# Performance work log

Measured on AMD Instinct MI355X. Metric: run time of the kernel, lower is better.

Reference implementation:

```python
import jax, jax.numpy as jnp
import numpy as np

N = 100000          # nodes
E = 1600000         # edges (avg degree 16)
F_IN = 128          # node_feature_dim
D = 64              # state_dim
LATENT = 32         # latent_dim -> output 2*latent
ROUNDS = 4


def setup_inputs() -> dict:
    key = jax.random.key(0)
    ks = jax.random.split(key, 12)
    s = 0.05  # weight scale
    return {
        "x": jax.random.normal(ks[0], (N, F_IN), dtype=jnp.float32),
        "edge_index": jax.random.randint(ks[1], (2, E), 0, N, dtype=jnp.int64),
        "batch": jnp.zeros((N,), dtype=jnp.int64),
        # input MLP: Linear(F_IN, D) + ReLU + Linear(D, D) + ReLU
        "W1": jax.random.normal(ks[2], (F_IN, D), dtype=jnp.float32) * s,
        "b1": jnp.zeros((D,), dtype=jnp.float32),
        "W2": jax.random.normal(ks[3], (D, D), dtype=jnp.float32) * s,
        "b2": jnp.zeros((D,), dtype=jnp.float32),
        # per-round GraphConv params (PyG: lin_rel has bias, lin_root does not)
        "Wrel": jax.random.normal(ks[4], (ROUNDS, D, D), dtype=jnp.float32) * s,
        "brel": jnp.zeros((ROUNDS, D), dtype=jnp.float32),
        "Wroot": jax.random.normal(ks[5], (ROUNDS, D, D), dtype=jnp.float32) * s,
        # output Linear(D, 2*latent)
        "Wout": jax.random.normal(ks[6], (D, 2 * LATENT), dtype=jnp.float32) * s,
        "bout": jnp.zeros((2 * LATENT,), dtype=jnp.float32),
    }


def reference(x, edge_index, batch, W1, b1, W2, b2, Wrel, brel, Wroot, Wout, bout):
    # input MLP (ends with ReLU) followed by the extra F.relu in forward (idempotent, kept for fidelity)
    h = jax.nn.relu(x @ W1 + b1)
    h = jax.nn.relu(h @ W2 + b2)
    h = jax.nn.relu(h)
    src, dst = edge_index[0], edge_index[1]
    n = h.shape[0]
    num_rounds = Wrel.shape[0]
    for r in range(num_rounds):
        # GraphConv: scatter-add of source features to destinations, then lin_rel + lin_root
        agg = jax.ops.segment_sum(h[src], dst, num_segments=n)  # [N, D]
        conv = agg @ Wrel[r] + brel[r] + h @ Wroot[r]
        h = h + jax.nn.relu(conv)  # residual
    return h @ Wout + bout  # [N, 2*latent]
```

## Files before the change

kernel.cpp:

```cpp
#include <hip/hip_runtime.h>
#include <hip/hip_bf16.h>

#define CAP 64
#define NPASS 4
#define WP 72
#define WP1 136

typedef __attribute__((ext_vector_type(8))) short bf16x8;
typedef __attribute__((ext_vector_type(4))) float f32x4;

__device__ __forceinline__ unsigned short f2bf(float f)
{
    __hip_bfloat16 t = __float2bfloat16(f);
    return *(unsigned short*)&t;
}

__device__ __forceinline__ bf16x8 cvt8(const float* s)
{
    bf16x8 r;
    #pragma unroll
    for (int i = 0; i < 8; ++i) r[i] = (short)f2bf(s[i]);
    return r;
}

__device__ __forceinline__ void acc8(float* a, float m, uint4 v)
{
    const unsigned u[4] = {v.x, v.y, v.z, v.w};
    #pragma unroll
    for (int i = 0; i < 4; ++i) {
        const float lo = __uint_as_float(u[i] << 16);
        const float hi = __uint_as_float(u[i] & 0xffff0000u);
        a[2 * i]     = fmaf(m, lo, a[2 * i]);
        a[2 * i + 1] = fmaf(m, hi, a[2 * i + 1]);
    }
}

__global__ void k_fillp(const int* __restrict__ ei, int* __restrict__ deg,
                        int* __restrict__ colp, int E, int lo, int hi)
{
    int e = blockIdx.x * 256 + threadIdx.x;
    if (e < E) {
        int dst = ei[E + e];
        if (dst >= lo && dst < hi) {
            int pos = atomicAdd(&deg[dst], 1);
            if (pos < CAP) colp[(size_t)dst * CAP + pos] = ei[e];
        }
    }
}

__global__ __launch_bounds__(256) void k_gather(
    const unsigned short* __restrict__ hb, unsigned short* __restrict__ aggb,
    const int* __restrict__ colp, const int* __restrict__ deg, int n)
{
    const int w = threadIdx.x >> 6, lane = threadIdx.x & 63;
    const int r = lane >> 3, c = lane & 7;
    const int node = blockIdx.x * 4 + w;
    if (node >= n) return;
    const int cnt = min(deg[node], CAP);

    float a[8], b[8];
    #pragma unroll
    for (int i = 0; i < 8; ++i) { a[i] = 0.f; b[i] = 0.f; }

    const int* cb = &colp[(size_t)node * CAP];
    for (int jb = 0; jb < cnt; jb += 16) {
        const int e0 = jb + r, e1 = jb + 8 + r;
        const int i0 = (e0 < cnt) ? cb[e0] : 0;
        const int i1 = (e1 < cnt) ? cb[e1] : 0;
        const float m0 = (e0 < cnt) ? 1.f : 0.f;
        const float m1 = (e1 < cnt) ? 1.f : 0.f;
        const uint4 v0 = *(const uint4*)&hb[(size_t)i0 * 64 + c * 8];
        const uint4 v1 = *(const uint4*)&hb[(size_t)i1 * 64 + c * 8];
        acc8(a, m0, v0);
        acc8(b, m1, v1);
    }
    #pragma unroll
    for (int i = 0; i < 8; ++i) {
        float s = a[i] + b[i];
        s += __shfl_xor(s, 8);
        s += __shfl_xor(s, 16);
        s += __shfl_xor(s, 32);
        a[i] = s;
    }
    if (r == 0) {
        uint4 q;
        q.x = ((unsigned)f2bf(a[1]) << 16) | f2bf(a[0]);
        q.y = ((unsigned)f2bf(a[3]) << 16) | f2bf(a[2]);
        q.z = ((unsigned)f2bf(a[5]) << 16) | f2bf(a[4]);
        q.w = ((unsigned)f2bf(a[7]) << 16) | f2bf(a[6]);
        *(uint4*)&aggb[(size_t)node * 64 + c * 8] = q;
    }
}


__global__ __launch_bounds__(256) void k_mlp_mfma(
    const float* __restrict__ x,
    const float* __restrict__ W1, const float* __restrict__ b1,
    const float* __restrict__ W2, const float* __restrict__ b2,
    float* __restrict__ h, unsigned short* __restrict__ hbf, int n)
{
    __shared__ unsigned short W1T[64 * WP1];
    __shared__ unsigned short W2T[64 * WP];
    __shared__ unsigned short t1[4][16 * WP];
    __shared__ float b1s[64], b2s[64];

    const int tid = threadIdx.x;
    for (int i = tid; i < 128 * 64; i += 256) {
        const int k = i >> 6, c = i & 63;
        W1T[c * WP1 + k] = f2bf(W1[i]);
    }
    for (int i = tid; i < 64 * 64; i += 256) {
        const int k = i >> 6, c = i & 63;
        W2T[c * WP + k] = f2bf(W2[i]);
    }
    if (tid < 64) { b1s[tid] = b1[tid]; b2s[tid] = b2[tid]; }
    __syncthreads();

    const int w = tid >> 6, l = tid & 63;
    const int lr = l & 15, lk = l >> 4;
    const int koff = lk * 8;
    const int ntile = (n + 63) >> 6;
    unsigned short* T = t1[w];

    for (int t = blockIdx.x; t < ntile; t += gridDim.x) {
        const int row0 = t * 64 + w * 16;
        const size_t xrow = (size_t)min(row0 + lr, n - 1) * 128;
        bf16x8 aX[4];
        #pragma unroll
        for (int kb = 0; kb < 4; ++kb) {
            float xf[8];
            *(float4*)&xf[0] = *(const float4*)&x[xrow + kb * 32 + koff];
            *(float4*)&xf[4] = *(const float4*)&x[xrow + kb * 32 + koff + 4];
            aX[kb] = cvt8(xf);
        }
        #pragma unroll
        for (int ni = 0; ni < 4; ++ni) {
            const int c = ni * 16 + lr;
            const float bias = b1s[c];
            f32x4 acc = {bias, bias, bias, bias};
            #pragma unroll
            for (int kb = 0; kb < 4; ++kb) {
                const bf16x8 bW = *(const bf16x8*)&W1T[c * WP1 + kb * 32 + koff];
                acc = __builtin_amdgcn_mfma_f32_16x16x32_bf16(aX[kb], bW, acc, 0, 0, 0);
            }
            #pragma unroll
            for (int r = 0; r < 4; ++r)
                T[(lk * 4 + r) * WP + c] = f2bf(fmaxf(acc[r], 0.f));
        }
        const bf16x8 aH0 = *(const bf16x8*)&T[lr * WP + koff];
        const bf16x8 aH1 = *(const bf16x8*)&T[lr * WP + 32 + koff];
        #pragma unroll
        for (int ni = 0; ni < 4; ++ni) {
            const int c = ni * 16 + lr;
            const float bias = b2s[c];
            f32x4 acc = {bias, bias, bias, bias};
            const bf16x8 b0 = *(const bf16x8*)&W2T[c * WP + koff];
            const bf16x8 b1f = *(const bf16x8*)&W2T[c * WP + 32 + koff];
            acc = __builtin_amdgcn_mfma_f32_16x16x32_bf16(aH0, b0, acc, 0, 0, 0);
            acc = __builtin_amdgcn_mfma_f32_16x16x32_bf16(aH1, b1f, acc, 0, 0, 0);
            #pragma unroll
            for (int r = 0; r < 4; ++r) {
                const int row = row0 + lk * 4 + r;
                if (row < n) {
                    const float v = fmaxf(acc[r], 0.f);
                    const size_t idx = (size_t)row * 64 + c;
                    h[idx] = v;
                    hbf[idx] = f2bf(v);
                }
            }
        }
    }
}

__global__ __launch_bounds__(256) void k_round_mfma(
    const unsigned short* __restrict__ aggb,
    unsigned short* hbf,
    float* h,
    const float* __restrict__ Wrel, const float* __restrict__ brel,
    const float* __restrict__ Wroot, int n)
{
    __shared__ unsigned short WrT[64 * WP];
    __shared__ unsigned short WoT[64 * WP];
    __shared__ float bs[64];
    const int tid = threadIdx.x;
    for (int i = tid; i < 4096; i += 256) {
        const int k = i >> 6, c = i & 63;
        WrT[c * WP + k] = f2bf(Wrel[i]);
        WoT[c * WP + k] = f2bf(Wroot[i]);
    }
    if (tid < 64) bs[tid] = brel[tid];
    __syncthreads();

    const int w = tid >> 6, l = tid & 63;
    const int lr = l & 15, lk = l >> 4;
    const int koff = lk * 8;
    const int ntile = (n + 63) >> 6;

    for (int t = blockIdx.x; t < ntile; t += gridDim.x) {
        const int row0 = t * 64 + w * 16;
        const size_t mrow = (size_t)min(row0 + lr, n - 1) * 64;
        const bf16x8 aA0 = *(const bf16x8*)&aggb[mrow + koff];
        const bf16x8 aA1 = *(const bf16x8*)&aggb[mrow + 32 + koff];
        const bf16x8 aH0 = *(const bf16x8*)&hbf [mrow + koff];
        const bf16x8 aH1 = *(const bf16x8*)&hbf [mrow + 32 + koff];
        #pragma unroll
        for (int ni = 0; ni < 4; ++ni) {
            const int c = ni * 16 + lr;
            const float bias = bs[c];
            f32x4 acc = {bias, bias, bias, bias};
            const bf16x8 br0 = *(const bf16x8*)&WrT[c * WP + koff];
            const bf16x8 br1 = *(const bf16x8*)&WrT[c * WP + 32 + koff];
            const bf16x8 bo0 = *(const bf16x8*)&WoT[c * WP + koff];
            const bf16x8 bo1 = *(const bf16x8*)&WoT[c * WP + 32 + koff];
            acc = __builtin_amdgcn_mfma_f32_16x16x32_bf16(aA0, br0, acc, 0, 0, 0);
            acc = __builtin_amdgcn_mfma_f32_16x16x32_bf16(aA1, br1, acc, 0, 0, 0);
            acc = __builtin_amdgcn_mfma_f32_16x16x32_bf16(aH0, bo0, acc, 0, 0, 0);
            acc = __builtin_amdgcn_mfma_f32_16x16x32_bf16(aH1, bo1, acc, 0, 0, 0);
            #pragma unroll
            for (int r = 0; r < 4; ++r) {
                const int row = row0 + lk * 4 + r;
                if (row < n) {
                    const size_t idx = (size_t)row * 64 + c;
                    const float v = h[idx] + fmaxf(acc[r], 0.f);
                    h[idx] = v;
                    hbf[idx] = f2bf(v);
                }
            }
        }
    }
}

__global__ __launch_bounds__(256) void k_out_mfma(
    const unsigned short* __restrict__ hbf,
    const float* __restrict__ Wout, const float* __restrict__ bout,
    float* __restrict__ out, int n)
{
    __shared__ unsigned short WT[64 * WP];
    __shared__ float bs[64];
    const int tid = threadIdx.x;
    for (int i = tid; i < 4096; i += 256) {
        const int k = i >> 6, c = i & 63;
        WT[c * WP + k] = f2bf(Wout[i]);
    }
    if (tid < 64) bs[tid] = bout[tid];
    __syncthreads();

    const int w = tid >> 6, l = tid & 63;
    const int lr = l & 15, lk = l >> 4;
    const int koff = lk * 8;
    const int ntile = (n + 63) >> 6;

    for (int t = blockIdx.x; t < ntile; t += gridDim.x) {
        const int row0 = t * 64 + w * 16;
        const size_t mrow = (size_t)min(row0 + lr, n - 1) * 64;
        const bf16x8 a0 = *(const bf16x8*)&hbf[mrow + koff];
        const bf16x8 a1 = *(const bf16x8*)&hbf[mrow + 32 + koff];
        #pragma unroll
        for (int ni = 0; ni < 4; ++ni) {
            const int c = ni * 16 + lr;
            const float bias = bs[c];
            f32x4 acc = {bias, bias, bias, bias};
            const bf16x8 b0 = *(const bf16x8*)&WT[c * WP + koff];
            const bf16x8 b1 = *(const bf16x8*)&WT[c * WP + 32 + koff];
            acc = __builtin_amdgcn_mfma_f32_16x16x32_bf16(a0, b0, acc, 0, 0, 0);
            acc = __builtin_amdgcn_mfma_f32_16x16x32_bf16(a1, b1, acc, 0, 0, 0);
            #pragma unroll
            for (int r = 0; r < 4; ++r) {
                const int row = row0 + lk * 4 + r;
                if (row < n) out[(size_t)row * 64 + c] = acc[r];
            }
        }
    }
}

extern "C" void kernel_launch(void* const* d_in, const int* in_sizes, int n_in,
                              void* d_out, int out_size, void* d_ws, size_t ws_size,
                              hipStream_t stream)
{
    const float* x    = (const float*)d_in[0];
    const int*   ei   = (const int*)  d_in[1];
    const float* W1   = (const float*)d_in[3];
    const float* b1   = (const float*)d_in[4];
    const float* W2   = (const float*)d_in[5];
    const float* b2   = (const float*)d_in[6];
    const float* Wrel = (const float*)d_in[7];
    const float* brel = (const float*)d_in[8];
    const float* Wroot= (const float*)d_in[9];
    const float* Wout = (const float*)d_in[10];
    const float* bout = (const float*)d_in[11];

    const int n = in_sizes[0] / 128;
    const int E = in_sizes[1] / 2;
    const int R = in_sizes[7] / (64 * 64);

    char* p = (char*)d_ws;
    float*          h    = (float*)p;          p += (size_t)n * 64 * sizeof(float);
    unsigned short* hbf  = (unsigned short*)p; p += (size_t)n * 64 * sizeof(unsigned short);
    unsigned short* aggb = (unsigned short*)p; p += (size_t)n * 64 * sizeof(unsigned short);
    int*            deg  = (int*)p;            p += (size_t)n * sizeof(int);
    int*            colp = (int*)p;            p += (size_t)n * CAP * sizeof(int);
    (void)ws_size; (void)n_in; (void)out_size;

    const int ebl = (E + 255) / 256;

    hipMemsetAsync(deg, 0, (size_t)n * sizeof(int), stream);
    for (int ps = 0; ps < NPASS; ++ps) {
        const int lo = (int)((long)n * ps / NPASS);
        const int hi = (int)((long)n * (ps + 1) / NPASS);
        k_fillp<<<ebl, 256, 0, stream>>>(ei, deg, colp, E, lo, hi);
    }

    k_mlp_mfma<<<1024, 256, 0, stream>>>(x, W1, b1, W2, b2, h, hbf, n);

    for (int r = 0; r < R; ++r) {
        k_gather<<<(n + 3) / 4, 256, 0, stream>>>(hbf, aggb, colp, deg, n);
        k_round_mfma<<<1024, 256, 0, stream>>>(
            aggb, hbf, h,
            Wrel + (size_t)r * 64 * 64, brel + (size_t)r * 64,
            Wroot + (size_t)r * 64 * 64, n);
    }

    k_out_mfma<<<1024, 256, 0, stream>>>(hbf, Wout, bout, (float*)d_out, n);
}
```

Measured before the change: 387.1 us.

## Switch to fp16 storage, drop fp32 residual copy, sentinel-pad gather

Node states are stored only as fp16 and the MFMAs switch from bf16 to f16, removing the separate fp32 h array and its per-round read/write traffic. The gather accumulates neighbour rows with packed fp16 vector adds and shuffles instead of fp32 FMAs with masks. Unused adjacency slots are prefilled with a sentinel index pointing at a zero row, so loads need no masking. This costs an extra init pass over the adjacency buffer and lowers precision of both the residual stream and the neighbour sum.

```diff
diff --git a/kernel.cpp b/kernel.cpp
--- a/kernel.cpp
+++ b/kernel.cpp
@@ -6,33 +6,17 @@
 #define WP 72
 #define WP1 136
 
-typedef __attribute__((ext_vector_type(8))) short bf16x8;
+typedef __attribute__((ext_vector_type(8))) _Float16 f16x8;
 typedef __attribute__((ext_vector_type(4))) float f32x4;
 
-__device__ __forceinline__ unsigned short f2bf(float f)
-{
-    __hip_bfloat16 t = __float2bfloat16(f);
-    return *(unsigned short*)&t;
-}
-
-__device__ __forceinline__ bf16x8 cvt8(const float* s)
-{
-    bf16x8 r;
-    #pragma unroll
-    for (int i = 0; i < 8; ++i) r[i] = (short)f2bf(s[i]);
-    return r;
-}
-
-__device__ __forceinline__ void acc8(float* a, float m, uint4 v)
-{
-    const unsigned u[4] = {v.x, v.y, v.z, v.w};
-    #pragma unroll
-    for (int i = 0; i < 4; ++i) {
-        const float lo = __uint_as_float(u[i] << 16);
-        const float hi = __uint_as_float(u[i] & 0xffff0000u);
-        a[2 * i]     = fmaf(m, lo, a[2 * i]);
-        a[2 * i + 1] = fmaf(m, hi, a[2 * i + 1]);
-    }
+__global__ void k_init(int4* __restrict__ colp4, _Float16* __restrict__ hh,
+                       int total4, int n)
+{
+    const int i = blockIdx.x * 256 + threadIdx.x;
+    const int4 v = {n, n, n, n};
+    for (int j = i; j < total4; j += gridDim.x * 256) colp4[j] = v;
+    if (blockIdx.x == 0 && threadIdx.x < 64)
+        hh[(size_t)n * 64 + threadIdx.x] = (_Float16)0.f;
 }
 
 __global__ void k_fillp(const int* __restrict__ ei, int* __restrict__ deg,
@@ -49,7 +33,7 @@
 }
 
 __global__ __launch_bounds__(256) void k_gather(
-    const unsigned short* __restrict__ hb, unsigned short* __restrict__ aggb,
+    const _Float16* __restrict__ hh, _Float16* __restrict__ aggh,
     const int* __restrict__ colp, const int* __restrict__ deg, int n)
 {
     const int w = threadIdx.x >> 6, lane = threadIdx.x & 63;
@@ -58,38 +42,26 @@
     if (node >= n) return;
     const int cnt = min(deg[node], CAP);
 
-    float a[8], b[8];
+    const int* cb = &colp[(size_t)node * CAP];
+    f16x8 s0 = {}; f16x8 s1 = {};
+    for (int jb = 0; jb < cnt; jb += 16) {
+        const int i0 = cb[jb + r];
+        const int i1 = cb[jb + 8 + r];
+        s0 += *(const f16x8*)&hh[(size_t)i0 * 64 + c * 8];
+        s1 += *(const f16x8*)&hh[(size_t)i1 * 64 + c * 8];
+    }
+    s0 += s1;
     #pragma unroll
-    for (int i = 0; i < 8; ++i) { a[i] = 0.f; b[i] = 0.f; }
-
-    const int* cb = &colp[(size_t)node * CAP];
-    for (int jb = 0; jb < cnt; jb += 16) {
-        const int e0 = jb + r, e1 = jb + 8 + r;
-        const int i0 = (e0 < cnt) ? cb[e0] : 0;
-        const int i1 = (e1 < cnt) ? cb[e1] : 0;
-        const float m0 = (e0 < cnt) ? 1.f : 0.f;
-        const float m1 = (e1 < cnt) ? 1.f : 0.f;
-        const uint4 v0 = *(const uint4*)&hb[(size_t)i0 * 64 + c * 8];
-        const uint4 v1 = *(const uint4*)&hb[(size_t)i1 * 64 + c * 8];
-        acc8(a, m0, v0);
-        acc8(b, m1, v1);
-    }
-    #pragma unroll
-    for (int i = 0; i < 8; ++i) {
-        float s = a[i] + b[i];
-        s += __shfl_xor(s, 8);
-        s += __shfl_xor(s, 16);
-        s += __shfl_xor(s, 32);
-        a[i] = s;
-    }
-    if (r == 0) {
-        uint4 q;
-        q.x = ((unsigned)f2bf(a[1]) << 16) | f2bf(a[0]);
-        q.y = ((unsigned)f2bf(a[3]) << 16) | f2bf(a[2]);
-        q.z = ((unsigned)f2bf(a[5]) << 16) | f2bf(a[4]);
-        q.w = ((unsigned)f2bf(a[7]) << 16) | f2bf(a[6]);
-        *(uint4*)&aggb[(size_t)node * 64 + c * 8] = q;
-    }
+    for (int st = 8; st <= 32; st <<= 1) {
+        uint4 u = *(uint4*)&s0, t;
+        t.x = __shfl_xor(u.x, st);
+        t.y = __shfl_xor(u.y, st);
+        t.z = __shfl_xor(u.z, st);
+        t.w = __shfl_xor(u.w, st);
+        s0 += *(f16x8*)&t;
+    }
+    if (r == 0)
+        *(uint4*)&aggh[(size_t)node * 64 + c * 8] = *(uint4*)&s0;
 }
 
 
@@ -97,21 +69,21 @@
     const float* __restrict__ x,
     const float* __restrict__ W1, const float* __restrict__ b1,
     const float* __restrict__ W2, const float* __restrict__ b2,
-    float* __restrict__ h, unsigned short* __restrict__ hbf, int n)
-{
-    __shared__ unsigned short W1T[64 * WP1];
-    __shared__ unsigned short W2T[64 * WP];
-    __shared__ unsigned short t1[4][16 * WP];
+    _Float16* __restrict__ hh, int n)
+{
+    __shared__ _Float16 W1T[64 * WP1];
+    __shared__ _Float16 W2T[64 * WP];
+    __shared__ _Float16 t1[4][16 * WP];
     __shared__ float b1s[64], b2s[64];
 
     const int tid = threadIdx.x;
     for (int i = tid; i < 128 * 64; i += 256) {
         const int k = i >> 6, c = i & 63;
-        W1T[c * WP1 + k] = f2bf(W1[i]);
+        W1T[c * WP1 + k] = (_Float16)W1[i];
     }
     for (int i = tid; i < 64 * 64; i += 256) {
         const int k = i >> 6, c = i & 63;
-        W2T[c * WP + k] = f2bf(W2[i]);
+        W2T[c * WP + k] = (_Float16)W2[i];
     }
     if (tid < 64) { b1s[tid] = b1[tid]; b2s[tid] = b2[tid]; }
     __syncthreads();
@@ -120,18 +92,21 @@
     const int lr = l & 15, lk = l >> 4;
     const int koff = lk * 8;
     const int ntile = (n + 63) >> 6;
-    unsigned short* T = t1[w];
+    _Float16* T = t1[w];
 
     for (int t = blockIdx.x; t < ntile; t += gridDim.x) {
         const int row0 = t * 64 + w * 16;
         const size_t xrow = (size_t)min(row0 + lr, n - 1) * 128;
-        bf16x8 aX[4];
+        f16x8 aX[4];
         #pragma unroll
         for (int kb = 0; kb < 4; ++kb) {
             float xf[8];
             *(float4*)&xf[0] = *(const float4*)&x[xrow + kb * 32 + koff];
             *(float4*)&xf[4] = *(const float4*)&x[xrow + kb * 32 + koff + 4];
-            aX[kb] = cvt8(xf);
+            f16x8 r;
+            #pragma unroll
+            for (int i = 0; i < 8; ++i) r[i] = (_Float16)xf[i];
+            aX[kb] = r;
         }
         #pragma unroll
         for (int ni = 0; ni < 4; ++ni) {
@@ -140,53 +115,48 @@
             f32x4 acc = {bias, bias, bias, bias};
             #pragma unroll
             for (int kb = 0; kb < 4; ++kb) {
-                const bf16x8 bW = *(const bf16x8*)&W1T[c * WP1 + kb * 32 + koff];
-                acc = __builtin_amdgcn_mfma_f32_16x16x32_bf16(aX[kb], bW, acc, 0, 0, 0);
+                const f16x8 bW = *(const f16x8*)&W1T[c * WP1 + kb * 32 + koff];
+                acc = __builtin_amdgcn_mfma_f32_16x16x32_f16(aX[kb], bW, acc, 0, 0, 0);
             }
             #pragma unroll
             for (int r = 0; r < 4; ++r)
-                T[(lk * 4 + r) * WP + c] = f2bf(fmaxf(acc[r], 0.f));
-        }
-        const bf16x8 aH0 = *(const bf16x8*)&T[lr * WP + koff];
-        const bf16x8 aH1 = *(const bf16x8*)&T[lr * WP + 32 + koff];
+                T[(lk * 4 + r) * WP + c] = (_Float16)fmaxf(acc[r], 0.f);
+        }
+        const f16x8 aH0 = *(const f16x8*)&T[lr * WP + koff];
+        const f16x8 aH1 = *(const f16x8*)&T[lr * WP + 32 + koff];
         #pragma unroll
         for (int ni = 0; ni < 4; ++ni) {
             const int c = ni * 16 + lr;
             const float bias = b2s[c];
             f32x4 acc = {bias, bias, bias, bias};
-            const bf16x8 b0 = *(const bf16x8*)&W2T[c * WP + koff];
-            const bf16x8 b1f = *(const bf16x8*)&W2T[c * WP + 32 + koff];
-            acc = __builtin_amdgcn_mfma_f32_16x16x32_bf16(aH0, b0, acc, 0, 0, 0);
-            acc = __builtin_amdgcn_mfma_f32_16x16x32_bf16(aH1, b1f, acc, 0, 0, 0);
+            const f16x8 b0 = *(const f16x8*)&W2T[c * WP + koff];
+            const f16x8 b1f = *(const f16x8*)&W2T[c * WP + 32 + koff];
+            acc = __builtin_amdgcn_mfma_f32_16x16x32_f16(aH0, b0, acc, 0, 0, 0);
+            acc = __builtin_amdgcn_mfma_f32_16x16x32_f16(aH1, b1f, acc, 0, 0, 0);
             #pragma unroll
             for (int r = 0; r < 4; ++r) {
                 const int row = row0 + lk * 4 + r;
-                if (row < n) {
-                    const float v = fmaxf(acc[r], 0.f);
-                    const size_t idx = (size_t)row * 64 + c;
-                    h[idx] = v;
-                    hbf[idx] = f2bf(v);
-                }
+                if (row < n)
+                    hh[(size_t)row * 64 + c] = (_Float16)fmaxf(acc[r], 0.f);
             }
         }
     }
 }
 
 __global__ __launch_bounds__(256) void k_round_mfma(
-    const unsigned short* __restrict__ aggb,
-    unsigned short* hbf,
-    float* h,
+    const _Float16* __restrict__ aggh,
+    _Float16* hh,
     const float* __restrict__ Wrel, const float* __restrict__ brel,
     const float* __restrict__ Wroot, int n)
 {
-    __shared__ unsigned short WrT[64 * WP];
-    __shared__ unsigned short WoT[64 * WP];
+    __shared__ _Float16 WrT[64 * WP];
+    __shared__ _Float16 WoT[64 * WP];
     __shared__ float bs[64];
     const int tid = threadIdx.x;
     for (int i = tid; i < 4096; i += 256) {
         const int k = i >> 6, c = i & 63;
-        WrT[c * WP + k] = f2bf(Wrel[i]);
-        WoT[c * WP + k] = f2bf(Wroot[i]);
+        WrT[c * WP + k] = (_Float16)Wrel[i];
+        WoT[c * WP + k] = (_Float16)Wroot[i];
     }
     if (tid < 64) bs[tid] = brel[tid];
     __syncthreads();
@@ -199,31 +169,30 @@
     for (int t = blockIdx.x; t < ntile; t += gridDim.x) {
         const int row0 = t * 64 + w * 16;
         const size_t mrow = (size_t)min(row0 + lr, n - 1) * 64;
-        const bf16x8 aA0 = *(const bf16x8*)&aggb[mrow + koff];
-        const bf16x8 aA1 = *(const bf16x8*)&aggb[mrow + 32 + koff];
-        const bf16x8 aH0 = *(const bf16x8*)&hbf [mrow + koff];
-        const bf16x8 aH1 = *(const bf16x8*)&hbf [mrow + 32 + koff];
+        const f16x8 aA0 = *(const f16x8*)&aggh[mrow + koff];
+        const f16x8 aA1 = *(const f16x8*)&aggh[mrow + 32 + koff];
+        const f16x8 aH0 = *(const f16x8*)&hh  [mrow + koff];
+        const f16x8 aH1 = *(const f16x8*)&hh  [mrow + 32 + koff];
         #pragma unroll
         for (int ni = 0; ni < 4; ++ni) {
             const int c = ni * 16 + lr;
             const float bias = bs[c];
             f32x4 acc = {bias, bias, bias, bias};
-            const bf16x8 br0 = *(const bf16x8*)&WrT[c * WP + koff];
-            const bf16x8 br1 = *(const bf16x8*)&WrT[c * WP + 32 + koff];
-            const bf16x8 bo0 = *(const bf16x8*)&WoT[c * WP + koff];
-            const bf16x8 bo1 = *(const bf16x8*)&WoT[c * WP + 32 + koff];
-            acc = __builtin_amdgcn_mfma_f32_16x16x32_bf16(aA0, br0, acc, 0, 0, 0);
-            acc = __builtin_amdgcn_mfma_f32_16x16x32_bf16(aA1, br1, acc, 0, 0, 0);
-            acc = __builtin_amdgcn_mfma_f32_16x16x32_bf16(aH0, bo0, acc, 0, 0, 0);
-            acc = __builtin_amdgcn_mfma_f32_16x16x32_bf16(aH1, bo1, acc, 0, 0, 0);
+            const f16x8 br0 = *(const f16x8*)&WrT[c * WP + koff];
+            const f16x8 br1 = *(const f16x8*)&WrT[c * WP + 32 + koff];
+            const f16x8 bo0 = *(const f16x8*)&WoT[c * WP + koff];
+            const f16x8 bo1 = *(const f16x8*)&WoT[c * WP + 32 + koff];
+            acc = __builtin_amdgcn_mfma_f32_16x16x32_f16(aA0, br0, acc, 0, 0, 0);
+            acc = __builtin_amdgcn_mfma_f32_16x16x32_f16(aA1, br1, acc, 0, 0, 0);
+            acc = __builtin_amdgcn_mfma_f32_16x16x32_f16(aH0, bo0, acc, 0, 0, 0);
+            acc = __builtin_amdgcn_mfma_f32_16x16x32_f16(aH1, bo1, acc, 0, 0, 0);
             #pragma unroll
             for (int r = 0; r < 4; ++r) {
                 const int row = row0 + lk * 4 + r;
                 if (row < n) {
                     const size_t idx = (size_t)row * 64 + c;
-                    const float v = h[idx] + fmaxf(acc[r], 0.f);
-                    h[idx] = v;
-                    hbf[idx] = f2bf(v);
+                    const float v = (float)hh[idx] + fmaxf(acc[r], 0.f);
+                    hh[idx] = (_Float16)v;
                 }
             }
         }
@@ -231,16 +200,16 @@
 }
 
 __global__ __launch_bounds__(256) void k_out_mfma(
-    const unsigned short* __restrict__ hbf,
+    const _Float16* __restrict__ hh,
     const float* __restrict__ Wout, const float* __restrict__ bout,
     float* __restrict__ out, int n)
 {
-    __shared__ unsigned short WT[64 * WP];
+    __shared__ _Float16 WT[64 * WP];
     __shared__ float bs[64];
     const int tid = threadIdx.x;
     for (int i = tid; i < 4096; i += 256) {
         const int k = i >> 6, c = i & 63;
-        WT[c * WP + k] = f2bf(Wout[i]);
+        WT[c * WP + k] = (_Float16)Wout[i];
     }
     if (tid < 64) bs[tid] = bout[tid];
     __syncthreads();
@@ -253,17 +222,17 @@
     for (int t = blockIdx.x; t < ntile; t += gridDim.x) {
         const int row0 = t * 64 + w * 16;
         const size_t mrow = (size_t)min(row0 + lr, n - 1) * 64;
-        const bf16x8 a0 = *(const bf16x8*)&hbf[mrow + koff];
-        const bf16x8 a1 = *(const bf16x8*)&hbf[mrow + 32 + koff];
+        const f16x8 a0 = *(const f16x8*)&hh[mrow + koff];
+        const f16x8 a1 = *(const f16x8*)&hh[mrow + 32 + koff];
         #pragma unroll
         for (int ni = 0; ni < 4; ++ni) {
             const int c = ni * 16 + lr;
             const float bias = bs[c];
             f32x4 acc = {bias, bias, bias, bias};
-            const bf16x8 b0 = *(const bf16x8*)&WT[c * WP + koff];
-            const bf16x8 b1 = *(const bf16x8*)&WT[c * WP + 32 + koff];
-            acc = __builtin_amdgcn_mfma_f32_16x16x32_bf16(a0, b0, acc, 0, 0, 0);
-            acc = __builtin_amdgcn_mfma_f32_16x16x32_bf16(a1, b1, acc, 0, 0, 0);
+            const f16x8 b0 = *(const f16x8*)&WT[c * WP + koff];
+            const f16x8 b1 = *(const f16x8*)&WT[c * WP + 32 + koff];
+            acc = __builtin_amdgcn_mfma_f32_16x16x32_f16(a0, b0, acc, 0, 0, 0);
+            acc = __builtin_amdgcn_mfma_f32_16x16x32_f16(a1, b1, acc, 0, 0, 0);
             #pragma unroll
             for (int r = 0; r < 4; ++r) {
                 const int row = row0 + lk * 4 + r;
@@ -294,15 +263,15 @@
     const int R = in_sizes[7] / (64 * 64);
 
     char* p = (char*)d_ws;
-    float*          h    = (float*)p;          p += (size_t)n * 64 * sizeof(float);
-    unsigned short* hbf  = (unsigned short*)p; p += (size_t)n * 64 * sizeof(unsigned short);
-    unsigned short* aggb = (unsigned short*)p; p += (size_t)n * 64 * sizeof(unsigned short);
-    int*            deg  = (int*)p;            p += (size_t)n * sizeof(int);
-    int*            colp = (int*)p;            p += (size_t)n * CAP * sizeof(int);
+    _Float16* hh   = (_Float16*)p; p += (size_t)(n + 1) * 64 * sizeof(_Float16);
+    _Float16* aggh = (_Float16*)p; p += (size_t)n * 64 * sizeof(_Float16);
+    int*      deg  = (int*)p;      p += (size_t)n * sizeof(int);
+    int*      colp = (int*)p;      p += (size_t)n * CAP * sizeof(int);
     (void)ws_size; (void)n_in; (void)out_size;
 
     const int ebl = (E + 255) / 256;
 
+    k_init<<<2048, 256, 0, stream>>>((int4*)colp, hh, n * (CAP / 4), n);
     hipMemsetAsync(deg, 0, (size_t)n * sizeof(int), stream);
     for (int ps = 0; ps < NPASS; ++ps) {
         const int lo = (int)((long)n * ps / NPASS);
@@ -310,15 +279,15 @@
         k_fillp<<<ebl, 256, 0, stream>>>(ei, deg, colp, E, lo, hi);
     }
 
-    k_mlp_mfma<<<1024, 256, 0, stream>>>(x, W1, b1, W2, b2, h, hbf, n);
+    k_mlp_mfma<<<1024, 256, 0, stream>>>(x, W1, b1, W2, b2, hh, n);
 
     for (int r = 0; r < R; ++r) {
-        k_gather<<<(n + 3) / 4, 256, 0, stream>>>(hbf, aggb, colp, deg, n);
+        k_gather<<<(n + 3) / 4, 256, 0, stream>>>(hh, aggh, colp, deg, n);
         k_round_mfma<<<1024, 256, 0, stream>>>(
-            aggb, hbf, h,
+            aggh, hh,
             Wrel + (size_t)r * 64 * 64, brel + (size_t)r * 64,
             Wroot + (size_t)r * 64 * 64, n);
     }
 
-    k_out_mfma<<<1024, 256, 0, stream>>>(hbf, Wout, bout, (float*)d_out, n);
-}
+    k_out_mfma<<<1024, 256, 0, stream>>>(hh, Wout, bout, (float*)d_out, n);
+}
```

New measurement: 334.7 us. -13.5%, faster.
